# Kernel optimization log

Hardware: AMD Instinct MI355X
Metric: run time of the kernel (lower is better)

Reference implementation:

```python
import jax, jax.numpy as jnp
import numpy as np

# Fused MPJRDLayer forward: all n_neurons processed in one batched pass.
# Neuron math (MPJRD spiking neuron, reconstructed from the layer contract):
#   dendritic/somatic integration: v[b,n] = sum_{d,s} x[b,n,d,s] * W[n,d,s]
#   spike: s[b,n] = 1[v >= theta[n]]   (Heaviside, surrogate-sigmoid gradient)
#   spike_rate[n] = mean_b s[b,n]
#   r_hat' = (1-ALPHA)*r_hat + ALPHA*rate   (homeostatic EMA)
#   theta' = theta + THETA_LR*(r_hat' - R_TARGET)  (threshold adaptation)
ALPHA = 0.05      # EMA rate for r_hat
THETA_LR = 0.1    # threshold adaptation rate
R_TARGET = 0.1    # target firing rate
SURR_K = 10.0     # surrogate gradient sharpness


def _spike(v, theta):
    u = v - theta[None, :]
    hard = (u >= 0).astype(v.dtype)
    soft = jax.nn.sigmoid(SURR_K * u)
    # forward == hard threshold, backward == sigmoid surrogate
    return jax.lax.stop_gradient(hard - soft) + soft


def setup_inputs() -> dict:
    key = jax.random.key(0)
    k1, k2, k3, k4 = jax.random.split(key, 4)
    B, N, D, S = 128, 1024, 8, 64
    x = jax.random.normal(k1, (B, N, D, S), dtype=jnp.float32)
    W = jax.random.normal(k2, (N, D, S), dtype=jnp.float32) / np.sqrt(D * S)
    theta = jax.random.uniform(k3, (N,), dtype=jnp.float32)
    r_hat = jax.random.uniform(k4, (N,), dtype=jnp.float32) * 0.2
    return {"x": x, "W": W, "theta": theta, "r_hat": r_hat}


def reference(x, W, theta, r_hat):
    # v: [B, N] somatic potential (fuses all per-neuron submodule calls)
    v = jnp.einsum("bnds,nds->bn", x, W)
    spikes = _spike(v, theta)                        # [B, N]
    rates = spikes.mean(axis=0)                      # [N]
    r_hats = (1.0 - ALPHA) * r_hat + ALPHA * rates   # [N]
    thetas = theta + THETA_LR * (r_hats - R_TARGET)  # [N]
    return spikes, rates, thetas, r_hats
```

## Files before the change

### kernel.cpp

```cpp
#include <hip/hip_runtime.h>

constexpr int B  = 128;
constexpr int N  = 1024;
constexpr int DS = 512;
constexpr int WPN = 8;
constexpr int BPW = B / WPN;

typedef float f32x4 __attribute__((ext_vector_type(4)));

__global__ __launch_bounds__(256) void mpjrd_spike_kernel(
    const float* __restrict__ x,
    const float* __restrict__ W,
    const float* __restrict__ theta,
    float*       __restrict__ out,
    float*       __restrict__ partial)
{
    const int tid  = threadIdx.x;
    const int lane = tid & 63;
    const int w    = blockIdx.x * 4 + (tid >> 6);
    const int n    = w >> 3;
    const int g    = w & 7;

    const size_t wbase = (size_t)n * DS + (size_t)lane * 4;
    const f32x4 w0 = *reinterpret_cast<const f32x4*>(W + wbase);
    const f32x4 w1 = *reinterpret_cast<const f32x4*>(W + wbase + 256);
    const double th = (double)theta[n];

    float cnt = 0.0f;
    const int b0 = g * BPW;

    #pragma unroll 4
    for (int i = 0; i < BPW; ++i) {
        const int b = b0 + i;
        const float* xp = x + ((size_t)b * N + n) * DS + (size_t)lane * 4;
        const f32x4 x0 = __builtin_nontemporal_load(reinterpret_cast<const f32x4*>(xp));
        const f32x4 x1 = __builtin_nontemporal_load(reinterpret_cast<const f32x4*>(xp + 256));

        double acc = (double)x0.x * (double)w0.x;
        acc += (double)x0.y * (double)w0.y;
        acc += (double)x0.z * (double)w0.z;
        acc += (double)x0.w * (double)w0.w;
        acc += (double)x1.x * (double)w1.x;
        acc += (double)x1.y * (double)w1.y;
        acc += (double)x1.z * (double)w1.z;
        acc += (double)x1.w * (double)w1.w;

        #pragma unroll
        for (int off = 32; off > 0; off >>= 1)
            acc += __shfl_down(acc, off);

        if (lane == 0) {
            const float s = (acc >= th) ? 1.0f : 0.0f;
            out[(size_t)b * N + n] = s;
            cnt += s;
        }
    }
    if (lane == 0) partial[n * WPN + g] = cnt;
}

__global__ __launch_bounds__(256) void mpjrd_finalize_kernel(
    const float* __restrict__ partial,
    const float* __restrict__ theta,
    const float* __restrict__ r_hat,
    float*       __restrict__ out)
{
    const int n = blockIdx.x * 256 + threadIdx.x;
    float c = 0.0f;
    #pragma unroll
    for (int i = 0; i < WPN; ++i) c += partial[n * WPN + i];
    const float rate = c * (1.0f / 128.0f);
    const float rh   = 0.95f * r_hat[n] + 0.05f * rate;
    const float th   = theta[n] + 0.1f * (rh - 0.1f);
    out[(size_t)B * N + n]         = rate;
    out[(size_t)B * N + N + n]     = th;
    out[(size_t)B * N + 2 * N + n] = rh;
}

extern "C" void kernel_launch(void* const* d_in, const int* in_sizes, int n_in,
                              void* d_out, int out_size, void* d_ws, size_t ws_size,
                              hipStream_t stream) {
    const float* x     = (const float*)d_in[0];
    const float* W     = (const float*)d_in[1];
    const float* theta = (const float*)d_in[2];
    const float* r_hat = (const float*)d_in[3];
    float* out     = (float*)d_out;
    float* partial = (float*)d_ws;

    mpjrd_spike_kernel<<<(N * WPN) / 4, 256, 0, stream>>>(x, W, theta, out, partial);
    mpjrd_finalize_kernel<<<N / 256, 256, 0, stream>>>(partial, theta, r_hat, out);
}
```

Before: 49.38 us.

## Retile spike kernel: each wave handles one batch row over eight neurons

Measured after the change: 47.54 us. 3.7% less time.

```diff
diff --git a/kernel.cpp b/kernel.cpp
--- a/kernel.cpp
+++ b/kernel.cpp
@@ -1,10 +1,12 @@
 #include <hip/hip_runtime.h>
 
-constexpr int B  = 128;
-constexpr int N  = 1024;
-constexpr int DS = 512;
-constexpr int WPN = 8;
-constexpr int BPW = B / WPN;
+constexpr int B   = 128;
+constexpr int N   = 1024;
+constexpr int DS  = 512;
+constexpr int NC  = 8;
+constexpr int NCH = N / NC;
+constexpr int BQ  = 4;
+constexpr int NBQ = B / BQ;
 
 typedef float f32x4 __attribute__((ext_vector_type(4)));
 
@@ -15,47 +17,66 @@
     float*       __restrict__ out,
     float*       __restrict__ partial)
 {
+    __shared__ float Wl[NC * DS];
+    __shared__ float thl[NC];
+    __shared__ float s_cnt[BQ][NC];
+
     const int tid  = threadIdx.x;
     const int lane = tid & 63;
-    const int w    = blockIdx.x * 4 + (tid >> 6);
-    const int n    = w >> 3;
-    const int g    = w & 7;
+    const int g    = tid >> 6;
+    const int nc   = blockIdx.x & (NCH - 1);
+    const int bq   = blockIdx.x >> 7;
+    const int n0   = nc * NC;
+    const int b    = bq * BQ + g;
 
-    const size_t wbase = (size_t)n * DS + (size_t)lane * 4;
-    const f32x4 w0 = *reinterpret_cast<const f32x4*>(W + wbase);
-    const f32x4 w1 = *reinterpret_cast<const f32x4*>(W + wbase + 256);
-    const double th = (double)theta[n];
+    {
+        const f32x4* Wg = reinterpret_cast<const f32x4*>(W + (size_t)n0 * DS);
+        f32x4* Wd = reinterpret_cast<f32x4*>(Wl);
+        #pragma unroll
+        for (int r = 0; r < 4; ++r) Wd[tid + r * 256] = Wg[tid + r * 256];
+        if (tid < NC) thl[tid] = theta[n0 + tid];
+    }
+    __syncthreads();
 
-    float cnt = 0.0f;
-    const int b0 = g * BPW;
+    const float* xp0 = x + ((size_t)b * N + n0) * DS + (size_t)lane * 4;
+    float spk[NC];
 
-    #pragma unroll 4
-    for (int i = 0; i < BPW; ++i) {
-        const int b = b0 + i;
-        const float* xp = x + ((size_t)b * N + n) * DS + (size_t)lane * 4;
+    #pragma unroll
+    for (int j = 0; j < NC; ++j) {
+        const float* xp = xp0 + (size_t)j * DS;
         const f32x4 x0 = __builtin_nontemporal_load(reinterpret_cast<const f32x4*>(xp));
         const f32x4 x1 = __builtin_nontemporal_load(reinterpret_cast<const f32x4*>(xp + 256));
+        const f32x4 wa = *reinterpret_cast<const f32x4*>(Wl + j * DS + lane * 4);
+        const f32x4 wb = *reinterpret_cast<const f32x4*>(Wl + j * DS + lane * 4 + 256);
 
-        double acc = (double)x0.x * (double)w0.x;
-        acc += (double)x0.y * (double)w0.y;
-        acc += (double)x0.z * (double)w0.z;
-        acc += (double)x0.w * (double)w0.w;
-        acc += (double)x1.x * (double)w1.x;
-        acc += (double)x1.y * (double)w1.y;
-        acc += (double)x1.z * (double)w1.z;
-        acc += (double)x1.w * (double)w1.w;
+        double acc = (double)x0.x * (double)wa.x;
+        acc += (double)x0.y * (double)wa.y;
+        acc += (double)x0.z * (double)wa.z;
+        acc += (double)x0.w * (double)wa.w;
+        acc += (double)x1.x * (double)wb.x;
+        acc += (double)x1.y * (double)wb.y;
+        acc += (double)x1.z * (double)wb.z;
+        acc += (double)x1.w * (double)wb.w;
 
         #pragma unroll
         for (int off = 32; off > 0; off >>= 1)
             acc += __shfl_down(acc, off);
 
-        if (lane == 0) {
-            const float s = (acc >= th) ? 1.0f : 0.0f;
-            out[(size_t)b * N + n] = s;
-            cnt += s;
-        }
+        spk[j] = (acc >= (double)thl[j]) ? 1.0f : 0.0f;
     }
-    if (lane == 0) partial[n * WPN + g] = cnt;
+
+    if (lane == 0) {
+        f32x4* op = reinterpret_cast<f32x4*>(out + (size_t)b * N + n0);
+        op[0] = f32x4{spk[0], spk[1], spk[2], spk[3]};
+        op[1] = f32x4{spk[4], spk[5], spk[6], spk[7]};
+        #pragma unroll
+        for (int j = 0; j < NC; ++j) s_cnt[g][j] = spk[j];
+    }
+    __syncthreads();
+    if (tid < NC) {
+        partial[(size_t)bq * N + n0 + tid] =
+            s_cnt[0][tid] + s_cnt[1][tid] + s_cnt[2][tid] + s_cnt[3][tid];
+    }
 }
 
 __global__ __launch_bounds__(256) void mpjrd_finalize_kernel(
@@ -67,7 +88,7 @@
     const int n = blockIdx.x * 256 + threadIdx.x;
     float c = 0.0f;
     #pragma unroll
-    for (int i = 0; i < WPN; ++i) c += partial[n * WPN + i];
+    for (int i = 0; i < NBQ; ++i) c += partial[(size_t)i * N + n];
     const float rate = c * (1.0f / 128.0f);
     const float rh   = 0.95f * r_hat[n] + 0.05f * rate;
     const float th   = theta[n] + 0.1f * (rh - 0.1f);
@@ -86,6 +107,6 @@
     float* out     = (float*)d_out;
     float* partial = (float*)d_ws;
 
-    mpjrd_spike_kernel<<<(N * WPN) / 4, 256, 0, stream>>>(x, W, theta, out, partial);
+    mpjrd_spike_kernel<<<NBQ * NCH, 256, 0, stream>>>(x, W, theta, out, partial);
     mpjrd_finalize_kernel<<<N / 256, 256, 0, stream>>>(partial, theta, r_hat, out);
 }
```
